# Kernel tuning notes

Hardware: AMD Instinct MI355X
Metric: run time of the kernel (lower is better)

The kernel has to match this reference:

```python
import jax, jax.numpy as jnp
import numpy as np

B, T, OB, AC, OBL, ACL, W = 2048, 128, 64, 8, 32, 16, 64
DT = 0.05   # spacing of save times
K = 2       # fixed Dopri5 substeps per interval (step size = ode_dt0 = 0.025)


def _mlp2(x, W0, b0, W1, b1):
    # eqx.nn.MLP with depth=1: in -> width (relu) -> out (identity)
    return jax.nn.relu(x @ W0.T + b0) @ W1.T + b1


def setup_inputs() -> dict:
    key = jax.random.key(0)
    ks = jax.random.split(key, 10)
    def lin(k, o, i, scale=1.0):
        return (jax.random.normal(k, (o, i), jnp.float32) * (scale / np.sqrt(i))).astype(jnp.float32)
    return {
        "encW0": lin(ks[0], W, OB), "encb0": jnp.zeros((W,), jnp.float32),
        "encW1": lin(ks[1], OBL, W), "encb1": jnp.zeros((OBL,), jnp.float32),
        "acW0": lin(ks[2], W, AC), "acb0": jnp.zeros((W,), jnp.float32),
        "acW1": lin(ks[3], ACL, W), "acb1": jnp.zeros((ACL,), jnp.float32),
        "dynW0": lin(ks[4], W, OBL + ACL), "dynb0": jnp.zeros((W,), jnp.float32),
        "dynW1": lin(ks[5], OBL, W, 0.5), "dynb1": jnp.zeros((OBL,), jnp.float32),
        "decW0": lin(ks[6], W, OBL), "decb0": jnp.zeros((W,), jnp.float32),
        "decW1": lin(ks[7], OB, W), "decb1": jnp.zeros((OB,), jnp.float32),
        "ob": jax.random.normal(ks[8], (B, OB), jnp.float32),
        "acs": jax.random.normal(ks[9], (B, T, AC), jnp.float32),
        "times": jnp.tile(jnp.arange(T, dtype=jnp.float32) * DT, (B, 1)),
    }


def _dopri5_step(f, t, y, h):
    k1 = f(t, y)
    k2 = f(t + h * (1. / 5.), y + h * ((1. / 5.) * k1))
    k3 = f(t + h * (3. / 10.), y + h * ((3. / 40.) * k1 + (9. / 40.) * k2))
    k4 = f(t + h * (4. / 5.), y + h * ((44. / 45.) * k1 - (56. / 15.) * k2 + (32. / 9.) * k3))
    k5 = f(t + h * (8. / 9.), y + h * ((19372. / 6561.) * k1 - (25360. / 2187.) * k2
                                       + (64448. / 6561.) * k3 - (212. / 729.) * k4))
    k6 = f(t + h, y + h * ((9017. / 3168.) * k1 - (355. / 33.) * k2 + (46732. / 5247.) * k3
                           + (49. / 176.) * k4 - (5103. / 18656.) * k5))
    return y + h * ((35. / 384.) * k1 + (500. / 1113.) * k3 + (125. / 192.) * k4
                    - (2187. / 6784.) * k5 + (11. / 84.) * k6)


def reference(encW0, encb0, encW1, encb1, acW0, acb0, acW1, acb1,
              dynW0, dynb0, dynW1, dynb1, decW0, decb0, decW1, decb1,
              ob, acs, times):
    ac_latents = _mlp2(acs, acW0, acb0, acW1, acb1)   # (B, T, ACL)
    y0 = _mlp2(ob, encW0, encb0, encW1, encb1)        # (B, OBL)

    def single(y0_i, acl_i, t_i):
        n = t_i.shape[0]

        def f(t, y):
            # piecewise-constant action latent: index of save-interval containing t
            idx = jnp.clip(jnp.searchsorted(t_i, t, side='right') - 1, 0, n - 1)
            return _mlp2(jnp.concatenate([y, acl_i[idx]]), dynW0, dynb0, dynW1, dynb1)

        def interval(y, tt):
            t0, t1 = tt
            h = (t1 - t0) / K
            def sub(yc, j):
                return _dopri5_step(f, t0 + j * h, yc, h), None
            y, _ = jax.lax.scan(sub, y, jnp.arange(K, dtype=t_i.dtype))
            return y, y

        _, ys = jax.lax.scan(interval, y0_i, (t_i[:-1], t_i[1:]))
        return jnp.concatenate([y0_i[None], ys], axis=0)   # (T, OBL)

    ys = jax.vmap(single)(y0, ac_latents, times)            # (B, T, OBL)
    return _mlp2(ys, decW0, decb0, decW1, decb1)            # (B, T, OB)
```

## Files before the change

kernel.cpp:

```cpp
#include <hip/hip_runtime.h>

#define NB 2048
#define NT 128

typedef float v2f __attribute__((ext_vector_type(2)));

static __device__ __forceinline__ v2f pkfma(v2f a, v2f b, v2f c) {
#if __has_builtin(__builtin_elementwise_fma)
    return __builtin_elementwise_fma(a, b, c);
#else
    v2f r; r.x = fmaf(a.x, b.x, c.x); r.y = fmaf(a.y, b.y, c.y); return r;
#endif
}
static __device__ __forceinline__ v2f mkv2(float x, float y) { v2f r; r.x = x; r.y = y; return r; }

__global__ __launch_bounds__(256, 4) void acl_kernel(
    const float* __restrict__ acs, const float* __restrict__ acW0,
    const float* __restrict__ acb0, const float* __restrict__ acW1,
    const float* __restrict__ acb1, float* __restrict__ aclout)
{
    __shared__ float sW0[64 * 8];
    __shared__ float sW1[16 * 64];
    __shared__ float sB0[64];
    __shared__ float sB1[16];
    const int tid = threadIdx.x;
    for (int i = tid; i < 64 * 8; i += 256) sW0[i] = acW0[i];
    for (int i = tid; i < 16 * 64; i += 256) sW1[i] = acW1[i];
    if (tid < 64) sB0[tid] = acb0[tid];
    if (tid < 16) sB1[tid] = acb1[tid];
    __syncthreads();

    const int row = blockIdx.x * 256 + tid;
    const float4 x0 = *(const float4*)&acs[row * 8];
    const float4 x1 = *(const float4*)&acs[row * 8 + 4];

    float o[16];
    #pragma unroll
    for (int m = 0; m < 16; ++m) o[m] = sB1[m];

    #pragma unroll
    for (int jc = 0; jc < 16; ++jc) {
        float hq[4];
        #pragma unroll
        for (int u = 0; u < 4; ++u) {
            const int j = jc * 4 + u;
            const float4 wa = *(const float4*)&sW0[j * 8];
            const float4 wb = *(const float4*)&sW0[j * 8 + 4];
            float hv = sB0[j];
            hv = fmaf(x0.x, wa.x, hv); hv = fmaf(x0.y, wa.y, hv);
            hv = fmaf(x0.z, wa.z, hv); hv = fmaf(x0.w, wa.w, hv);
            hv = fmaf(x1.x, wb.x, hv); hv = fmaf(x1.y, wb.y, hv);
            hv = fmaf(x1.z, wb.z, hv); hv = fmaf(x1.w, wb.w, hv);
            hq[u] = fmaxf(hv, 0.f);
        }
        #pragma unroll
        for (int m = 0; m < 16; ++m) {
            const float4 wv = *(const float4*)&sW1[m * 64 + jc * 4];
            o[m] = fmaf(hq[0], wv.x, o[m]);
            o[m] = fmaf(hq[1], wv.y, o[m]);
            o[m] = fmaf(hq[2], wv.z, o[m]);
            o[m] = fmaf(hq[3], wv.w, o[m]);
        }
    }
    float4* op = (float4*)&aclout[row * 16];
    op[0] = make_float4(o[0],  o[1],  o[2],  o[3]);
    op[1] = make_float4(o[4],  o[5],  o[6],  o[7]);
    op[2] = make_float4(o[8],  o[9],  o[10], o[11]);
    op[3] = make_float4(o[12], o[13], o[14], o[15]);
}

__global__ __launch_bounds__(256, 2) void ode_kernel(
    const float* __restrict__ encW0, const float* __restrict__ encb0,
    const float* __restrict__ encW1, const float* __restrict__ encb1,
    const float* __restrict__ dynW0, const float* __restrict__ dynb0,
    const float* __restrict__ dynW1, const float* __restrict__ dynb1,
    const float* __restrict__ ob,    const float* __restrict__ times,
    const float* __restrict__ aclws, float* __restrict__ yio)
{
    __shared__ float sEncW0T[64 * 64];
    __shared__ float sEncW1T[64 * 32];
    __shared__ float sW0s[64 * 32];
    __shared__ float sW1T[64 * 32];
    __shared__ float sM[64 * 64];
    __shared__ float sEncB0[64], sEncB1[32], sB1d[32];
    __shared__ float xbuf[4][64];
    __shared__ float hbuf[4][64];
    __shared__ float tbuf[4][NT];

    const int tid = threadIdx.x;
    for (int i = tid; i < 64 * 64; i += 256) { int r = i >> 6, c = i & 63; sEncW0T[c * 64 + r] = encW0[i]; }
    for (int i = tid; i < 32 * 64; i += 256) { int r = i >> 6, c = i & 63; sEncW1T[c * 32 + r] = encW1[i]; }
    for (int i = tid; i < 64 * 32; i += 256) { int j = i >> 5, mm = i & 31; sW0s[i] = dynW0[j * 48 + mm]; }
    for (int i = tid; i < 64 * 32; i += 256) { int c = i >> 5, mm = i & 31; sW1T[i] = dynW1[mm * 64 + c]; }
    if (tid < 64) { sEncB0[tid] = encb0[tid]; }
    if (tid < 32) { sEncB1[tid] = encb1[tid]; sB1d[tid] = dynb1[tid]; }
    __syncthreads();

    {
        const int j  = tid >> 2;
        const int cg = (tid & 3) * 16;
        float4 wr[8];
        #pragma unroll
        for (int q = 0; q < 8; ++q) wr[q] = *(const float4*)&sW0s[j * 32 + q * 4];
        #pragma unroll 2
        for (int k = 0; k < 16; ++k) {
            const int c = cg + k;
            v2f s0 = mkv2(0.f, 0.f), s1 = mkv2(0.f, 0.f);
            #pragma unroll
            for (int q = 0; q < 8; ++q) {
                const float4 t4 = *(const float4*)&sW1T[c * 32 + q * 4];
                s0 = pkfma(mkv2(t4.x, t4.y), mkv2(wr[q].x, wr[q].y), s0);
                s1 = pkfma(mkv2(t4.z, t4.w), mkv2(wr[q].z, wr[q].w), s1);
            }
            sM[j * 64 + c] = (s0.x + s1.x) + (s0.y + s1.y);
        }
    }
    __syncthreads();

    const int w    = tid >> 6;
    const int lane = tid & 63;
    const int bu   = __builtin_amdgcn_readfirstlane(blockIdx.x * 4 + w);
    const int m    = lane & 31;
    const int H    = lane & 32;

    float* __restrict__ xb = xbuf[w];
    float* __restrict__ hb = hbuf[w];

    float w0r[48];
    #pragma unroll
    for (int q = 0; q < 12; ++q) *(float4*)&w0r[q * 4] = *(const float4*)&dynW0[lane * 48 + q * 4];
    float w1r[32];
    #pragma unroll
    for (int q = 0; q < 8; ++q)  *(float4*)&w1r[q * 4] = *(const float4*)&dynW1[m * 64 + H + q * 4];
    float Ma[32], Mb[32];
    #pragma unroll
    for (int q = 0; q < 8; ++q) *(float4*)&Ma[q * 4] = *(const float4*)&sM[lane * 64 + H + q * 4];
    #pragma unroll
    for (int q = 0; q < 8; ++q) *(float4*)&Mb[q * 4] = *(const float4*)&sM[(lane ^ 32) * 64 + H + q * 4];
    const float b0r = dynb0[lane];
    const float b1r = dynb1[m];

    float vj;
    {
        v2f s0 = mkv2(0.f, 0.f), s1 = mkv2(0.f, 0.f);
        const v2f* wp = (const v2f*)w0r;
        const v2f* bp = (const v2f*)sB1d;
        #pragma unroll
        for (int q = 0; q < 16; q += 2) {
            s0 = pkfma(bp[q],     wp[q],     s0);
            s1 = pkfma(bp[q + 1], wp[q + 1], s1);
        }
        vj = (s0.x + s1.x) + (s0.y + s1.y);
    }

    tbuf[w][lane]      = times[bu * NT + lane];
    tbuf[w][64 + lane] = times[bu * NT + 64 + lane];
    __builtin_amdgcn_wave_barrier();

    auto gproj = [&](float hsv) -> float {
        __builtin_amdgcn_wave_barrier();
        hb[lane] = hsv;
        __builtin_amdgcn_wave_barrier();
        float hr[32];
        #pragma unroll
        for (int q = 0; q < 8; ++q) *(float4*)&hr[q * 4] = *(const float4*)&hb[H + q * 4];
        const v2f* hp = (const v2f*)hr;
        const v2f* ma = (const v2f*)Ma;
        const v2f* mb = (const v2f*)Mb;
        v2f o0 = mkv2(0.f, 0.f), o1 = mkv2(0.f, 0.f);
        v2f p0 = mkv2(0.f, 0.f), p1 = mkv2(0.f, 0.f);
        #pragma unroll
        for (int q = 0; q < 16; q += 2) {
            o0 = pkfma(hp[q],     ma[q],     o0);
            o1 = pkfma(hp[q + 1], ma[q + 1], o1);
            p0 = pkfma(hp[q],     mb[q],     p0);
            p1 = pkfma(hp[q + 1], mb[q + 1], p1);
        }
        const float own = (o0.x + o1.x) + (o0.y + o1.y);
        float par = (p0.x + p1.x) + (p0.y + p1.y);
        par = __shfl_xor(par, 32, 64);
        return own + par + vj;
    };

    float y;
    {
        xb[lane] = ob[bu * 64 + lane];
        __builtin_amdgcn_wave_barrier();
        float4 xv[16];
        #pragma unroll
        for (int q = 0; q < 16; ++q) xv[q] = *(const float4*)&xb[q * 4];
        float a0 = sEncB0[lane], a1 = 0.f, a2 = 0.f, a3 = 0.f;
        #pragma unroll
        for (int q = 0; q < 16; ++q) {
            a0 = fmaf(xv[q].x, sEncW0T[(q * 4 + 0) * 64 + lane], a0);
            a1 = fmaf(xv[q].y, sEncW0T[(q * 4 + 1) * 64 + lane], a1);
            a2 = fmaf(xv[q].z, sEncW0T[(q * 4 + 2) * 64 + lane], a2);
            a3 = fmaf(xv[q].w, sEncW0T[(q * 4 + 3) * 64 + lane], a3);
        }
        const float hj = fmaxf((a0 + a1) + (a2 + a3), 0.f);
        hb[lane] = hj;
        __builtin_amdgcn_wave_barrier();
        float4 hv[8];
        #pragma unroll
        for (int q = 0; q < 8; ++q) hv[q] = *(const float4*)&hb[H + q * 4];
        float c0 = 0.f, c1 = 0.f, c2 = 0.f, c3 = 0.f;
        #pragma unroll
        for (int q = 0; q < 8; ++q) {
            c0 = fmaf(hv[q].x, sEncW1T[(H + q * 4 + 0) * 32 + m], c0);
            c1 = fmaf(hv[q].y, sEncW1T[(H + q * 4 + 1) * 32 + m], c1);
            c2 = fmaf(hv[q].z, sEncW1T[(H + q * 4 + 2) * 32 + m], c2);
            c3 = fmaf(hv[q].w, sEncW1T[(H + q * 4 + 3) * 32 + m], c3);
        }
        float part = (c0 + c1) + (c2 + c3);
        part += __shfl_xor(part, 32, 64);
        y = part + sEncB1[m];
    }

    auto acl_part = [&](const float* __restrict__ ap) -> float {
        float ar[16];
        #pragma unroll
        for (int q = 0; q < 4; ++q) *(float4*)&ar[q * 4] = *(const float4*)&ap[q * 4];
        const v2f* a2 = (const v2f*)ar;
        const v2f* wq = (const v2f*)&w0r[32];
        v2f s0 = mkv2(0.f, 0.f), s1 = mkv2(0.f, 0.f);
        #pragma unroll
        for (int q = 0; q < 8; q += 2) {
            s0 = pkfma(a2[q],     wq[q],     s0);
            s1 = pkfma(a2[q + 1], wq[q + 1], s1);
        }
        const v2f s = s0 + s1;
        return s.x + s.y;
    };

    auto store_y = [&](float yv, int t) {
        if (lane < 32) yio[(size_t)(bu * NT + t) * 64 + lane] = yv;
    };

    float aclPartC = acl_part(aclws + (size_t)(bu * NT) * 16);
    store_y(y, 0);

    for (int i = 0; i < NT - 1; ++i) {
        const float t0v = tbuf[w][i];
        const float t1v = tbuf[w][i + 1];
        const float hh  = (t1v - t0v) * 0.5f;
        const float aclPartN = acl_part(aclws + (size_t)(bu * NT + i + 1) * 16);

        #pragma unroll 1
        for (int sub = 0; sub < 2; ++sub) {
            const float tsub  = t0v + (float)sub * hh;
            const bool  swap6 = (tsub + hh >= t1v);

            __builtin_amdgcn_wave_barrier();
            xb[m] = y;
            __builtin_amdgcn_wave_barrier();
            float a1v;
            {
                float xr[32];
                #pragma unroll
                for (int q = 0; q < 8; ++q) *(float4*)&xr[q * 4] = *(const float4*)&xb[q * 4];
                const v2f* xp = (const v2f*)xr;
                const v2f* wp = (const v2f*)w0r;
                v2f s0 = mkv2(b0r + aclPartC, 0.f), s1 = mkv2(0.f, 0.f);
                #pragma unroll
                for (int q = 0; q < 16; q += 2) {
                    s0 = pkfma(xp[q],     wp[q],     s0);
                    s1 = pkfma(xp[q + 1], wp[q + 1], s1);
                }
                a1v = (s0.x + s1.x) + (s0.y + s1.y);
            }

            const float h1 = fmaxf(a1v, 0.f);
            const float g1 = hh * gproj(h1);
            const float h2 = fmaxf(fmaf(0.2f, g1, a1v), 0.f);
            const float g2 = hh * gproj(h2);
            const float h3 = fmaxf(fmaf(0.075f, g1, fmaf(0.225f, g2, a1v)), 0.f);
            const float g3 = hh * gproj(h3);
            const float h4 = fmaxf(
                fmaf((float)(44.0/45.0), g1,
                fmaf((float)(-56.0/15.0), g2,
                fmaf((float)(32.0/9.0), g3, a1v))), 0.f);
            const float g4 = hh * gproj(h4);
            const float h5 = fmaxf(
                fmaf((float)(19372.0/6561.0), g1,
                fmaf((float)(-25360.0/2187.0), g2,
                fmaf((float)(64448.0/6561.0), g3,
                fmaf((float)(-212.0/729.0), g4, a1v)))), 0.f);
            const float g5 = hh * gproj(h5);
            float a6v =
                fmaf((float)(9017.0/3168.0), g1,
                fmaf((float)(-355.0/33.0), g2,
                fmaf((float)(46732.0/5247.0), g3,
                fmaf((float)(49.0/176.0), g4,
                fmaf((float)(-5103.0/18656.0), g5, a1v)))));
            a6v += swap6 ? (aclPartN - aclPartC) : 0.f;
            const float h6 = fmaxf(a6v, 0.f);

            float ha = (float)(35.0/384.0) * h1;
            ha = fmaf((float)(500.0/1113.0),   h3, ha);
            ha = fmaf((float)(125.0/192.0),    h4, ha);
            ha = fmaf((float)(-2187.0/6784.0), h5, ha);
            ha = fmaf((float)(11.0/84.0),      h6, ha);

            __builtin_amdgcn_wave_barrier();
            hb[lane] = ha;
            __builtin_amdgcn_wave_barrier();
            {
                float hr[32];
                #pragma unroll
                for (int q = 0; q < 8; ++q) *(float4*)&hr[q * 4] = *(const float4*)&hb[H + q * 4];
                const v2f* hp  = (const v2f*)hr;
                const v2f* w1p = (const v2f*)w1r;
                v2f c0 = mkv2(0.f, 0.f), c1 = mkv2(0.f, 0.f);
                #pragma unroll
                for (int q = 0; q < 16; q += 2) {
                    c0 = pkfma(hp[q],     w1p[q],     c0);
                    c1 = pkfma(hp[q + 1], w1p[q + 1], c1);
                }
                float part = (c0.x + c1.x) + (c0.y + c1.y);
                part += __shfl_xor(part, 32, 64);
                y = fmaf(hh, part + b1r, y);
            }
        }
        aclPartC = aclPartN;
        store_y(y, i + 1);
    }
}

__global__ __launch_bounds__(256, 2) void dec_kernel(
    const float* __restrict__ decW0, const float* __restrict__ decb0,
    const float* __restrict__ decW1, const float* __restrict__ decb1,
    float* __restrict__ yio)
{
    __shared__ float sW0[64 * 32];
    __shared__ float sW1T[64 * 64];
    __shared__ float sB0[64];
    __shared__ float sB1[64];
    const int tid = threadIdx.x;
    for (int i = tid; i < 64 * 32; i += 256) sW0[i] = decW0[i];
    for (int i = tid; i < 64 * 64; i += 256) { int n = i >> 6, j = i & 63; sW1T[j * 64 + n] = decW1[i]; }
    if (tid < 64) { sB0[tid] = decb0[tid]; sB1[tid] = decb1[tid]; }
    __syncthreads();

    const size_t row = (size_t)blockIdx.x * 256 + tid;
    float* rp = &yio[row * 64];

    float xr[32];
    #pragma unroll
    for (int q = 0; q < 8; ++q) *(float4*)&xr[q * 4] = *(const float4*)&rp[q * 4];

    v2f o2[32];
    #pragma unroll
    for (int n = 0; n < 32; ++n) o2[n] = mkv2(sB1[2 * n], sB1[2 * n + 1]);

    #pragma unroll 4
    for (int j = 0; j < 64; ++j) {
        v2f a0 = mkv2(sB0[j], 0.f), a1 = mkv2(0.f, 0.f);
        #pragma unroll
        for (int q = 0; q < 8; ++q) {
            const float4 wv = *(const float4*)&sW0[j * 32 + q * 4];
            a0 = pkfma(*(const v2f*)&xr[q * 4],     mkv2(wv.x, wv.y), a0);
            a1 = pkfma(*(const v2f*)&xr[q * 4 + 2], mkv2(wv.z, wv.w), a1);
        }
        const float hj = fmaxf((a0.x + a1.x) + (a0.y + a1.y), 0.f);
        const v2f h2 = mkv2(hj, hj);
        #pragma unroll
        for (int q = 0; q < 16; ++q) {
            const float4 wv = *(const float4*)&sW1T[j * 64 + q * 4];
            o2[2 * q]     = pkfma(h2, mkv2(wv.x, wv.y), o2[2 * q]);
            o2[2 * q + 1] = pkfma(h2, mkv2(wv.z, wv.w), o2[2 * q + 1]);
        }
    }

    #pragma unroll
    for (int q = 0; q < 16; ++q)
        *(float4*)&rp[q * 4] = make_float4(o2[2 * q].x, o2[2 * q].y,
                                           o2[2 * q + 1].x, o2[2 * q + 1].y);
}

extern "C" void kernel_launch(void* const* d_in, const int* in_sizes, int n_in,
                              void* d_out, int out_size, void* d_ws, size_t ws_size,
                              hipStream_t stream)
{
    const float* encW0 = (const float*)d_in[0];
    const float* encb0 = (const float*)d_in[1];
    const float* encW1 = (const float*)d_in[2];
    const float* encb1 = (const float*)d_in[3];
    const float* acW0  = (const float*)d_in[4];
    const float* acb0  = (const float*)d_in[5];
    const float* acW1  = (const float*)d_in[6];
    const float* acb1  = (const float*)d_in[7];
    const float* dynW0 = (const float*)d_in[8];
    const float* dynb0 = (const float*)d_in[9];
    const float* dynW1 = (const float*)d_in[10];
    const float* dynb1 = (const float*)d_in[11];
    const float* decW0 = (const float*)d_in[12];
    const float* decb0 = (const float*)d_in[13];
    const float* decW1 = (const float*)d_in[14];
    const float* decb1 = (const float*)d_in[15];
    const float* ob    = (const float*)d_in[16];
    const float* acs   = (const float*)d_in[17];
    const float* times = (const float*)d_in[18];
    float* out = (float*)d_out;
    float* acl = (float*)d_ws;

    acl_kernel<<<(NB * NT) / 256, 256, 0, stream>>>(acs, acW0, acb0, acW1, acb1, acl);
    ode_kernel<<<NB / 4, 256, 0, stream>>>(encW0, encb0, encW1, encb1,
                                           dynW0, dynb0, dynW1, dynb1,
                                           ob, times, acl, out);
    dec_kernel<<<(NB * NT) / 256, 256, 0, stream>>>(decW0, decb0, decW1, decb1, out);
}
```

Baseline: 614.1 us.

## Track pre-activation state and use DPP lane gathers instead of LDS round-trips

The solver now carries the projected state W0·y (ystar) instead of y. Each substep updates it through the fused W0·W1 matrix applied to the Dopri5-weighted hidden vector, so the per-substep W0 matvec and its LDS write/read disappear. y itself is rebuilt once per interval from the summed hidden vectors via W1. The hidden-vector broadcast for each matvec now uses DPP quad, half-mirror and mirror permutes plus a few xor shuffles instead of LDS stores and barriers, with the weight registers pre-permuted to match. This raises register pressure (four 16-element v2f weight sets) and changes floating-point summation order.

```diff
diff --git a/kernel.cpp b/kernel.cpp
--- a/kernel.cpp
+++ b/kernel.cpp
@@ -13,6 +13,16 @@
 #endif
 }
 static __device__ __forceinline__ v2f mkv2(float x, float y) { v2f r; r.x = x; r.y = y; return r; }
+
+template<int CTRL>
+static __device__ __forceinline__ float dppf(float v) {
+    return __int_as_float(__builtin_amdgcn_update_dpp(
+        __float_as_int(v), __float_as_int(v), CTRL, 0xF, 0xF, false));
+}
+#define DPP_QP1 0xB1
+#define DPP_QP2 0x4E
+#define DPP_HM  0x141
+#define DPP_MIR 0x140
 
 __global__ __launch_bounds__(256, 4) void acl_kernel(
     const float* __restrict__ acs, const float* __restrict__ acW0,
@@ -122,64 +132,70 @@
     const int bu   = __builtin_amdgcn_readfirstlane(blockIdx.x * 4 + w);
     const int m    = lane & 31;
     const int H    = lane & 32;
+    const int rb   = lane & 48;
+    const int off  = lane & 15;
 
     float* __restrict__ xb = xbuf[w];
     float* __restrict__ hb = hbuf[w];
 
-    float w0r[48];
-    #pragma unroll
-    for (int q = 0; q < 12; ++q) *(float4*)&w0r[q * 4] = *(const float4*)&dynW0[lane * 48 + q * 4];
-    float w1r[32];
-    #pragma unroll
-    for (int q = 0; q < 8; ++q)  *(float4*)&w1r[q * 4] = *(const float4*)&dynW1[m * 64 + H + q * 4];
-    float Ma[32], Mb[32];
-    #pragma unroll
-    for (int q = 0; q < 8; ++q) *(float4*)&Ma[q * 4] = *(const float4*)&sM[lane * 64 + H + q * 4];
-    #pragma unroll
-    for (int q = 0; q < 8; ++q) *(float4*)&Mb[q * 4] = *(const float4*)&sM[(lane ^ 32) * 64 + H + q * 4];
+    constexpr int XT[8][2] = {{0,1},{2,3},{7,6},{5,4},{15,14},{13,12},{8,9},{10,11}};
+
+    v2f WM0[8], WM1[8], WM2[8], WM3[8];
+    #pragma unroll
+    for (int q = 0; q < 8; ++q) {
+        const int c0 = rb | (off ^ XT[q][0]);
+        const int c1 = rb | (off ^ XT[q][1]);
+        WM0[q] = mkv2(sM[lane * 64 + c0],        sM[lane * 64 + c1]);
+        WM1[q] = mkv2(sM[(lane ^ 16) * 64 + c0], sM[(lane ^ 16) * 64 + c1]);
+        WM2[q] = mkv2(sM[(lane ^ 32) * 64 + c0], sM[(lane ^ 32) * 64 + c1]);
+        WM3[q] = mkv2(sM[(lane ^ 48) * 64 + c0], sM[(lane ^ 48) * 64 + c1]);
+    }
+    v2f V10[8], V11[8];
+    #pragma unroll
+    for (int q = 0; q < 8; ++q) {
+        const int c0 = rb | (off ^ XT[q][0]);
+        const int c1 = rb | (off ^ XT[q][1]);
+        V10[q] = mkv2(dynW1[m * 64 + c0],        dynW1[m * 64 + c1]);
+        V11[q] = mkv2(dynW1[(m ^ 16) * 64 + c0], dynW1[(m ^ 16) * 64 + c1]);
+    }
+    float wa[16];
+    #pragma unroll
+    for (int q = 0; q < 4; ++q) *(float4*)&wa[q * 4] = *(const float4*)&dynW0[lane * 48 + 32 + q * 4];
     const float b0r = dynb0[lane];
     const float b1r = dynb1[m];
-
-    float vj;
-    {
-        v2f s0 = mkv2(0.f, 0.f), s1 = mkv2(0.f, 0.f);
-        const v2f* wp = (const v2f*)w0r;
-        const v2f* bp = (const v2f*)sB1d;
-        #pragma unroll
-        for (int q = 0; q < 16; q += 2) {
-            s0 = pkfma(bp[q],     wp[q],     s0);
-            s1 = pkfma(bp[q + 1], wp[q + 1], s1);
-        }
-        vj = (s0.x + s1.x) + (s0.y + s1.y);
-    }
 
     tbuf[w][lane]      = times[bu * NT + lane];
     tbuf[w][64 + lane] = times[bu * NT + 64 + lane];
     __builtin_amdgcn_wave_barrier();
 
-    auto gproj = [&](float hsv) -> float {
-        __builtin_amdgcn_wave_barrier();
-        hb[lane] = hsv;
-        __builtin_amdgcn_wave_barrier();
-        float hr[32];
-        #pragma unroll
-        for (int q = 0; q < 8; ++q) *(float4*)&hr[q * 4] = *(const float4*)&hb[H + q * 4];
-        const v2f* hp = (const v2f*)hr;
-        const v2f* ma = (const v2f*)Ma;
-        const v2f* mb = (const v2f*)Mb;
-        v2f o0 = mkv2(0.f, 0.f), o1 = mkv2(0.f, 0.f);
-        v2f p0 = mkv2(0.f, 0.f), p1 = mkv2(0.f, 0.f);
-        #pragma unroll
-        for (int q = 0; q < 16; q += 2) {
-            o0 = pkfma(hp[q],     ma[q],     o0);
-            o1 = pkfma(hp[q + 1], ma[q + 1], o1);
-            p0 = pkfma(hp[q],     mb[q],     p0);
-            p1 = pkfma(hp[q + 1], mb[q + 1], p1);
-        }
-        const float own = (o0.x + o1.x) + (o0.y + o1.y);
-        float par = (p0.x + p1.x) + (p0.y + p1.y);
-        par = __shfl_xor(par, 32, 64);
-        return own + par + vj;
+    auto gather = [&](float h, v2f* G) {
+        G[0] = mkv2(h,                     dppf<DPP_QP1>(h));
+        G[1] = mkv2(dppf<DPP_QP2>(G[0].x), dppf<DPP_QP2>(G[0].y));
+        G[2] = mkv2(dppf<DPP_HM >(G[0].x), dppf<DPP_HM >(G[0].y));
+        G[3] = mkv2(dppf<DPP_HM >(G[1].x), dppf<DPP_HM >(G[1].y));
+        G[4] = mkv2(dppf<DPP_MIR>(G[0].x), dppf<DPP_MIR>(G[0].y));
+        G[5] = mkv2(dppf<DPP_MIR>(G[1].x), dppf<DPP_MIR>(G[1].y));
+        G[6] = mkv2(dppf<DPP_MIR>(G[2].x), dppf<DPP_MIR>(G[2].y));
+        G[7] = mkv2(dppf<DPP_MIR>(G[3].x), dppf<DPP_MIR>(G[3].y));
+    };
+
+    auto gproj = [&](float h, float vjv) -> float {
+        v2f G[8];
+        gather(h, G);
+        v2f P0 = mkv2(0.f, 0.f), P1 = mkv2(0.f, 0.f);
+        v2f P2 = mkv2(0.f, 0.f), P3 = mkv2(0.f, 0.f);
+        #pragma unroll
+        for (int q = 0; q < 8; ++q) {
+            P0 = pkfma(G[q], WM0[q], P0);
+            P1 = pkfma(G[q], WM1[q], P1);
+            P2 = pkfma(G[q], WM2[q], P2);
+            P3 = pkfma(G[q], WM3[q], P3);
+        }
+        const float p0 = P0.x + P0.y, p1 = P1.x + P1.y;
+        const float p2 = P2.x + P2.y, p3 = P3.x + P3.y;
+        const float u  = p0 + __shfl_xor(p1, 16, 64);
+        const float vv = p2 + __shfl_xor(p3, 16, 64);
+        return u + __shfl_xor(vv, 32, 64) + vjv;
     };
 
     float y;
@@ -216,12 +232,28 @@
         y = part + sEncB1[m];
     }
 
+    float ystar = 0.f, vj = 0.f;
+    {
+        __builtin_amdgcn_wave_barrier();
+        xb[m] = y;
+        __builtin_amdgcn_wave_barrier();
+        #pragma unroll
+        for (int q = 0; q < 8; ++q) {
+            const float4 wv = *(const float4*)&dynW0[lane * 48 + q * 4];
+            const float4 xv = *(const float4*)&xb[q * 4];
+            ystar = fmaf(wv.x, xv.x, ystar); ystar = fmaf(wv.y, xv.y, ystar);
+            ystar = fmaf(wv.z, xv.z, ystar); ystar = fmaf(wv.w, xv.w, ystar);
+            vj = fmaf(wv.x, sB1d[q * 4 + 0], vj); vj = fmaf(wv.y, sB1d[q * 4 + 1], vj);
+            vj = fmaf(wv.z, sB1d[q * 4 + 2], vj); vj = fmaf(wv.w, sB1d[q * 4 + 3], vj);
+        }
+    }
+
     auto acl_part = [&](const float* __restrict__ ap) -> float {
         float ar[16];
         #pragma unroll
         for (int q = 0; q < 4; ++q) *(float4*)&ar[q * 4] = *(const float4*)&ap[q * 4];
         const v2f* a2 = (const v2f*)ar;
-        const v2f* wq = (const v2f*)&w0r[32];
+        const v2f* wq = (const v2f*)wa;
         v2f s0 = mkv2(0.f, 0.f), s1 = mkv2(0.f, 0.f);
         #pragma unroll
         for (int q = 0; q < 8; q += 2) {
@@ -244,48 +276,32 @@
         const float t1v = tbuf[w][i + 1];
         const float hh  = (t1v - t0v) * 0.5f;
         const float aclPartN = acl_part(aclws + (size_t)(bu * NT + i + 1) * 16);
+        float haccS = 0.f;
 
         #pragma unroll 1
         for (int sub = 0; sub < 2; ++sub) {
             const float tsub  = t0v + (float)sub * hh;
             const bool  swap6 = (tsub + hh >= t1v);
 
-            __builtin_amdgcn_wave_barrier();
-            xb[m] = y;
-            __builtin_amdgcn_wave_barrier();
-            float a1v;
-            {
-                float xr[32];
-                #pragma unroll
-                for (int q = 0; q < 8; ++q) *(float4*)&xr[q * 4] = *(const float4*)&xb[q * 4];
-                const v2f* xp = (const v2f*)xr;
-                const v2f* wp = (const v2f*)w0r;
-                v2f s0 = mkv2(b0r + aclPartC, 0.f), s1 = mkv2(0.f, 0.f);
-                #pragma unroll
-                for (int q = 0; q < 16; q += 2) {
-                    s0 = pkfma(xp[q],     wp[q],     s0);
-                    s1 = pkfma(xp[q + 1], wp[q + 1], s1);
-                }
-                a1v = (s0.x + s1.x) + (s0.y + s1.y);
-            }
+            const float a1v = ystar + b0r + aclPartC;
 
             const float h1 = fmaxf(a1v, 0.f);
-            const float g1 = hh * gproj(h1);
+            const float g1 = hh * gproj(h1, vj);
             const float h2 = fmaxf(fmaf(0.2f, g1, a1v), 0.f);
-            const float g2 = hh * gproj(h2);
+            const float g2 = hh * gproj(h2, vj);
             const float h3 = fmaxf(fmaf(0.075f, g1, fmaf(0.225f, g2, a1v)), 0.f);
-            const float g3 = hh * gproj(h3);
+            const float g3 = hh * gproj(h3, vj);
             const float h4 = fmaxf(
                 fmaf((float)(44.0/45.0), g1,
                 fmaf((float)(-56.0/15.0), g2,
                 fmaf((float)(32.0/9.0), g3, a1v))), 0.f);
-            const float g4 = hh * gproj(h4);
+            const float g4 = hh * gproj(h4, vj);
             const float h5 = fmaxf(
                 fmaf((float)(19372.0/6561.0), g1,
                 fmaf((float)(-25360.0/2187.0), g2,
                 fmaf((float)(64448.0/6561.0), g3,
                 fmaf((float)(-212.0/729.0), g4, a1v)))), 0.f);
-            const float g5 = hh * gproj(h5);
+            const float g5 = hh * gproj(h5, vj);
             float a6v =
                 fmaf((float)(9017.0/3168.0), g1,
                 fmaf((float)(-355.0/33.0), g2,
@@ -301,25 +317,24 @@
             ha = fmaf((float)(-2187.0/6784.0), h5, ha);
             ha = fmaf((float)(11.0/84.0),      h6, ha);
 
-            __builtin_amdgcn_wave_barrier();
-            hb[lane] = ha;
-            __builtin_amdgcn_wave_barrier();
-            {
-                float hr[32];
-                #pragma unroll
-                for (int q = 0; q < 8; ++q) *(float4*)&hr[q * 4] = *(const float4*)&hb[H + q * 4];
-                const v2f* hp  = (const v2f*)hr;
-                const v2f* w1p = (const v2f*)w1r;
-                v2f c0 = mkv2(0.f, 0.f), c1 = mkv2(0.f, 0.f);
-                #pragma unroll
-                for (int q = 0; q < 16; q += 2) {
-                    c0 = pkfma(hp[q],     w1p[q],     c0);
-                    c1 = pkfma(hp[q + 1], w1p[q + 1], c1);
-                }
-                float part = (c0.x + c1.x) + (c0.y + c1.y);
-                part += __shfl_xor(part, 32, 64);
-                y = fmaf(hh, part + b1r, y);
+            const float gacc = gproj(ha, vj);
+            ystar = fmaf(hh, gacc, ystar);
+            haccS += ha;
+        }
+
+        {
+            v2f G[8];
+            gather(haccS, G);
+            v2f P0 = mkv2(0.f, 0.f), P1 = mkv2(0.f, 0.f);
+            #pragma unroll
+            for (int q = 0; q < 8; ++q) {
+                P0 = pkfma(G[q], V10[q], P0);
+                P1 = pkfma(G[q], V11[q], P1);
             }
+            const float p0 = P0.x + P0.y, p1 = P1.x + P1.y;
+            const float u  = p0 + __shfl_xor(p1, 16, 64);
+            const float gf = u + __shfl_xor(u, 32, 64);
+            y = fmaf(hh, gf + 2.f * b1r, y);
         }
         aclPartC = aclPartN;
         store_y(y, i + 1);
```

New measurement: 726.9 us. +18.4%, slower.

## Track projected state in hidden space and batch output projection per interval

Applied to the files above, without the earlier changes.

Keeps the first-layer projection of y (ystar = W0y·y) as a running per-lane value, updated each substep through the precomputed M = W0y·W1 matrix via gproj. This removes the per-substep LDS broadcast of y and the 32-wide dot product. It also accumulates both substeps' hidden combinations so the W1 output projection runs once per interval instead of twice. The 32-lane half-swap reductions now use permlane32_swap when available. The cost is one extra gproj per substep and possible floating-point drift, since ystar is no longer recomputed from y.

```diff
diff --git a/kernel.cpp b/kernel.cpp
--- a/kernel.cpp
+++ b/kernel.cpp
@@ -13,6 +13,16 @@
 #endif
 }
 static __device__ __forceinline__ v2f mkv2(float x, float y) { v2f r; r.x = x; r.y = y; return r; }
+
+static __device__ __forceinline__ float sum32(float p) {
+#if __has_builtin(__builtin_amdgcn_permlane32_swap)
+    typedef unsigned uv2 __attribute__((ext_vector_type(2)));
+    uv2 r = __builtin_amdgcn_permlane32_swap(__float_as_uint(p), __float_as_uint(p), false, false);
+    return __uint_as_float(r.x) + __uint_as_float(r.y);
+#else
+    return p + __shfl_xor(p, 32, 64);
+#endif
+}
 
 __global__ __launch_bounds__(256, 4) void acl_kernel(
     const float* __restrict__ acs, const float* __restrict__ acW0,
@@ -126,31 +136,29 @@
     float* __restrict__ xb = xbuf[w];
     float* __restrict__ hb = hbuf[w];
 
-    float w0r[48];
-    #pragma unroll
-    for (int q = 0; q < 12; ++q) *(float4*)&w0r[q * 4] = *(const float4*)&dynW0[lane * 48 + q * 4];
-    float w1r[32];
-    #pragma unroll
-    for (int q = 0; q < 8; ++q)  *(float4*)&w1r[q * 4] = *(const float4*)&dynW1[m * 64 + H + q * 4];
-    float Ma[32], Mb[32];
-    #pragma unroll
-    for (int q = 0; q < 8; ++q) *(float4*)&Ma[q * 4] = *(const float4*)&sM[lane * 64 + H + q * 4];
-    #pragma unroll
-    for (int q = 0; q < 8; ++q) *(float4*)&Mb[q * 4] = *(const float4*)&sM[(lane ^ 32) * 64 + H + q * 4];
+    float Maf[32], Mbf[32];
+    #pragma unroll
+    for (int q = 0; q < 8; ++q) *(float4*)&Maf[q * 4] = *(const float4*)&sM[lane * 64 + H + q * 4];
+    #pragma unroll
+    for (int q = 0; q < 8; ++q) *(float4*)&Mbf[q * 4] = *(const float4*)&sM[(lane ^ 32) * 64 + H + q * 4];
+    const v2f* Ma = (const v2f*)Maf;
+    const v2f* Mb = (const v2f*)Mbf;
+    float w1rf[32];
+    #pragma unroll
+    for (int q = 0; q < 8; ++q)  *(float4*)&w1rf[q * 4] = *(const float4*)&dynW1[m * 64 + H + q * 4];
+    const v2f* w1r = (const v2f*)w1rf;
+    float wa[16];
+    #pragma unroll
+    for (int q = 0; q < 4; ++q) *(float4*)&wa[q * 4] = *(const float4*)&dynW0[lane * 48 + 32 + q * 4];
     const float b0r = dynb0[lane];
     const float b1r = dynb1[m];
 
-    float vj;
-    {
-        v2f s0 = mkv2(0.f, 0.f), s1 = mkv2(0.f, 0.f);
-        const v2f* wp = (const v2f*)w0r;
-        const v2f* bp = (const v2f*)sB1d;
-        #pragma unroll
-        for (int q = 0; q < 16; q += 2) {
-            s0 = pkfma(bp[q],     wp[q],     s0);
-            s1 = pkfma(bp[q + 1], wp[q + 1], s1);
-        }
-        vj = (s0.x + s1.x) + (s0.y + s1.y);
+    float vj = 0.f;
+    #pragma unroll
+    for (int q = 0; q < 8; ++q) {
+        const float4 wv = *(const float4*)&dynW0[lane * 48 + q * 4];
+        vj = fmaf(wv.x, sB1d[q * 4 + 0], vj); vj = fmaf(wv.y, sB1d[q * 4 + 1], vj);
+        vj = fmaf(wv.z, sB1d[q * 4 + 2], vj); vj = fmaf(wv.w, sB1d[q * 4 + 3], vj);
     }
 
     tbuf[w][lane]      = times[bu * NT + lane];
@@ -165,21 +173,19 @@
         #pragma unroll
         for (int q = 0; q < 8; ++q) *(float4*)&hr[q * 4] = *(const float4*)&hb[H + q * 4];
         const v2f* hp = (const v2f*)hr;
-        const v2f* ma = (const v2f*)Ma;
-        const v2f* mb = (const v2f*)Mb;
-        v2f o0 = mkv2(0.f, 0.f), o1 = mkv2(0.f, 0.f);
-        v2f p0 = mkv2(0.f, 0.f), p1 = mkv2(0.f, 0.f);
+        v2f O0 = mkv2(0.f, 0.f), O1 = mkv2(0.f, 0.f);
+        v2f P0 = mkv2(0.f, 0.f), P1 = mkv2(0.f, 0.f);
         #pragma unroll
         for (int q = 0; q < 16; q += 2) {
-            o0 = pkfma(hp[q],     ma[q],     o0);
-            o1 = pkfma(hp[q + 1], ma[q + 1], o1);
-            p0 = pkfma(hp[q],     mb[q],     p0);
-            p1 = pkfma(hp[q + 1], mb[q + 1], p1);
-        }
-        const float own = (o0.x + o1.x) + (o0.y + o1.y);
-        float par = (p0.x + p1.x) + (p0.y + p1.y);
-        par = __shfl_xor(par, 32, 64);
-        return own + par + vj;
+            O0 = pkfma(hp[q],     Ma[q],     O0);
+            O1 = pkfma(hp[q + 1], Ma[q + 1], O1);
+            P0 = pkfma(hp[q],     Mb[q],     P0);
+            P1 = pkfma(hp[q + 1], Mb[q + 1], P1);
+        }
+        const float own = (O0.x + O1.x) + (O0.y + O1.y);
+        const float par = (P0.x + P1.x) + (P0.y + P1.y);
+        const float s = own + par, d = own - par;
+        return fmaf(0.5f, sum32(s) - sum32(d), d) + vj;
     };
 
     float y;
@@ -211,9 +217,22 @@
             c2 = fmaf(hv[q].z, sEncW1T[(H + q * 4 + 2) * 32 + m], c2);
             c3 = fmaf(hv[q].w, sEncW1T[(H + q * 4 + 3) * 32 + m], c3);
         }
-        float part = (c0 + c1) + (c2 + c3);
-        part += __shfl_xor(part, 32, 64);
-        y = part + sEncB1[m];
+        const float part = (c0 + c1) + (c2 + c3);
+        y = sum32(part) + sEncB1[m];
+    }
+
+    float ystar = 0.f;
+    {
+        __builtin_amdgcn_wave_barrier();
+        xb[m] = y;
+        __builtin_amdgcn_wave_barrier();
+        #pragma unroll
+        for (int q = 0; q < 8; ++q) {
+            const float4 wv = *(const float4*)&dynW0[lane * 48 + q * 4];
+            const float4 xv = *(const float4*)&xb[q * 4];
+            ystar = fmaf(wv.x, xv.x, ystar); ystar = fmaf(wv.y, xv.y, ystar);
+            ystar = fmaf(wv.z, xv.z, ystar); ystar = fmaf(wv.w, xv.w, ystar);
+        }
     }
 
     auto acl_part = [&](const float* __restrict__ ap) -> float {
@@ -221,7 +240,7 @@
         #pragma unroll
         for (int q = 0; q < 4; ++q) *(float4*)&ar[q * 4] = *(const float4*)&ap[q * 4];
         const v2f* a2 = (const v2f*)ar;
-        const v2f* wq = (const v2f*)&w0r[32];
+        const v2f* wq = (const v2f*)wa;
         v2f s0 = mkv2(0.f, 0.f), s1 = mkv2(0.f, 0.f);
         #pragma unroll
         for (int q = 0; q < 8; q += 2) {
@@ -244,30 +263,14 @@
         const float t1v = tbuf[w][i + 1];
         const float hh  = (t1v - t0v) * 0.5f;
         const float aclPartN = acl_part(aclws + (size_t)(bu * NT + i + 1) * 16);
+        float haccS = 0.f;
 
         #pragma unroll 1
         for (int sub = 0; sub < 2; ++sub) {
             const float tsub  = t0v + (float)sub * hh;
             const bool  swap6 = (tsub + hh >= t1v);
 
-            __builtin_amdgcn_wave_barrier();
-            xb[m] = y;
-            __builtin_amdgcn_wave_barrier();
-            float a1v;
-            {
-                float xr[32];
-                #pragma unroll
-                for (int q = 0; q < 8; ++q) *(float4*)&xr[q * 4] = *(const float4*)&xb[q * 4];
-                const v2f* xp = (const v2f*)xr;
-                const v2f* wp = (const v2f*)w0r;
-                v2f s0 = mkv2(b0r + aclPartC, 0.f), s1 = mkv2(0.f, 0.f);
-                #pragma unroll
-                for (int q = 0; q < 16; q += 2) {
-                    s0 = pkfma(xp[q],     wp[q],     s0);
-                    s1 = pkfma(xp[q + 1], wp[q + 1], s1);
-                }
-                a1v = (s0.x + s1.x) + (s0.y + s1.y);
-            }
+            const float a1v = ystar + b0r + aclPartC;
 
             const float h1 = fmaxf(a1v, 0.f);
             const float g1 = hh * gproj(h1);
@@ -301,25 +304,28 @@
             ha = fmaf((float)(-2187.0/6784.0), h5, ha);
             ha = fmaf((float)(11.0/84.0),      h6, ha);
 
+            const float gacc = gproj(ha);
+            ystar = fmaf(hh, gacc, ystar);
+            haccS += ha;
+        }
+
+        {
             __builtin_amdgcn_wave_barrier();
-            hb[lane] = ha;
+            hb[lane] = haccS;
             __builtin_amdgcn_wave_barrier();
-            {
-                float hr[32];
-                #pragma unroll
-                for (int q = 0; q < 8; ++q) *(float4*)&hr[q * 4] = *(const float4*)&hb[H + q * 4];
-                const v2f* hp  = (const v2f*)hr;
-                const v2f* w1p = (const v2f*)w1r;
-                v2f c0 = mkv2(0.f, 0.f), c1 = mkv2(0.f, 0.f);
-                #pragma unroll
-                for (int q = 0; q < 16; q += 2) {
-                    c0 = pkfma(hp[q],     w1p[q],     c0);
-                    c1 = pkfma(hp[q + 1], w1p[q + 1], c1);
-                }
-                float part = (c0.x + c1.x) + (c0.y + c1.y);
-                part += __shfl_xor(part, 32, 64);
-                y = fmaf(hh, part + b1r, y);
+            float hr[32];
+            #pragma unroll
+            for (int q = 0; q < 8; ++q) *(float4*)&hr[q * 4] = *(const float4*)&hb[H + q * 4];
+            const v2f* hp = (const v2f*)hr;
+            v2f c0 = mkv2(0.f, 0.f), c1 = mkv2(0.f, 0.f);
+            #pragma unroll
+            for (int q = 0; q < 16; q += 2) {
+                c0 = pkfma(hp[q],     w1r[q],     c0);
+                c1 = pkfma(hp[q + 1], w1r[q + 1], c1);
             }
+            const float part = (c0.x + c1.x) + (c0.y + c1.y);
+            const float full = sum32(part);
+            y = fmaf(hh, full + 2.f * b1r, y);
         }
         aclPartC = aclPartN;
         store_y(y, i + 1);
```

Result: slower. 651.7 us (+6.1%).
